# Performance work log

Measured on AMD Instinct MI355X. Metric: run time of the kernel, lower is better.

## Reference

```python
import jax, jax.numpy as jnp
import numpy as np

P_W, P_H = 4, 8            # patch_size=[4,8]: p[0]=width, p[1]=height
EMBED, DEPTH, HEADS = 384, 12, 6
HD = EMBED // HEADS        # 64
THETA = 100.0
LN_EPS = 1e-5


def axial_freqs(pw, ph):
    # compute_axial_cis(dim=HD, end_x=pw, end_y=ph): angles for x and y axes, as cos/sin
    f = 1.0 / THETA ** (np.arange(0, HD, 4)[: HD // 4].astype(np.float32) / HD)  # (16,)
    t = np.arange(pw * ph, dtype=np.float32)
    tx, ty = t % pw, np.floor(t / pw)
    ang = np.concatenate([np.outer(tx, f), np.outer(ty, f)], -1)  # (N, 32)
    return jnp.asarray(np.cos(ang)), jnp.asarray(np.sin(ang))


def patchify(img):
    # (3, h, w) -> (ph*pw, 3*P_H*P_W), matching view/permute in NaViT_ROPE.forward
    c, h, w = img.shape
    ph, pw = h // P_H, w // P_W
    seq = img.reshape(c, ph, P_H, pw, P_W).transpose(1, 3, 0, 2, 4).reshape(ph * pw, -1)
    return seq, ph, pw


def layer_norm(x, w, b):
    m = x.mean(-1, keepdims=True)
    v = ((x - m) ** 2).mean(-1, keepdims=True)
    return (x - m) / jnp.sqrt(v + LN_EPS) * w + b


def rope(x, cos, sin):
    # x: (B,H,N,HD) paired as (...,HD//2,2); cos/sin: (B,N,HD//2)
    xp = x.reshape(*x.shape[:-1], -1, 2)
    x0, x1 = xp[..., 0], xp[..., 1]
    c, s = cos[:, None], sin[:, None]
    return jnp.stack([x0 * c - x1 * s, x0 * s + x1 * c], -1).reshape(x.shape)


def forward(imgs, params):
    (pe_ln_in_w, pe_ln_in_b, pe_w, pe_ln_out_w, pe_ln_out_b, blk, lnf_w, lnf_b) = params
    seqs, coss, sins, lens = [], [], [], []
    for img in imgs:
        seq, ph, pw = patchify(img)
        c, s = axial_freqs(pw, ph)
        seqs.append(seq); coss.append(c); sins.append(s); lens.append(seq.shape[0])
    nmax = max(lens)
    pad = lambda a: jnp.pad(a, ((0, nmax - a.shape[0]), (0, 0)))
    x = jnp.stack([pad(s) for s in seqs])      # (B, Nmax, 96)
    cos = jnp.stack([pad(c) for c in coss])    # (B, Nmax, 32)
    sin = jnp.stack([pad(s) for s in sins])
    mask = jnp.arange(nmax)[None, :] >= jnp.array(lens)[:, None]        # (B, Nmax), True = pad
    attn_bias = jnp.where(mask, -jnp.inf, 0.0)[:, None, None, :]        # (B,1,1,Nmax)

    # patch embed: LN(96) -> Linear(96,384,no bias) -> LN(384)
    x = layer_norm(x, pe_ln_in_w, pe_ln_in_b) @ pe_w
    x = layer_norm(x, pe_ln_out_w, pe_ln_out_b)

    scale = HD ** -0.5

    def block(x, p):
        ln1_w, ln1_b, qkv_w, qkv_b, proj_w, proj_b, ln2_w, ln2_b, fc1_w, fc1_b, fc2_w, fc2_b = p
        B, N, C = x.shape
        h = layer_norm(x, ln1_w, ln1_b)
        qkv = (h @ qkv_w + qkv_b).reshape(B, N, 3, HEADS, HD).transpose(2, 0, 3, 1, 4)
        q, k, v = qkv[0], qkv[1], qkv[2]
        q, k = rope(q, cos, sin), rope(k, cos, sin)
        attn = jnp.einsum('bhnd,bhmd->bhnm', q * scale, k) + attn_bias
        attn = jax.nn.softmax(attn, axis=-1)
        o = jnp.einsum('bhnm,bhmd->bhnd', attn, v).transpose(0, 2, 1, 3).reshape(B, N, C)
        x = x + (o @ proj_w + proj_b)
        h2 = layer_norm(x, ln2_w, ln2_b)
        h2 = jax.nn.gelu(h2 @ fc1_w + fc1_b, approximate=False)  # torch nn.GELU default (erf)
        x = x + (h2 @ fc2_w + fc2_b)
        return x, None

    x, _ = jax.lax.scan(block, x, blk)
    x = layer_norm(x, lnf_w, lnf_b)
    return x, mask


def setup_inputs() -> dict:
    key = jax.random.key(0)
    ks = jax.random.split(key, 10)
    sizes = [(3, 32, 512), (3, 32, 768), (3, 32, 896), (3, 32, 1024)]
    pd = 3 * P_H * P_W  # 96
    w = lambda k, sh: jax.random.normal(k, sh, jnp.float32) * 0.02
    inp = {}
    for i, s in enumerate(sizes):
        inp[f'img{i}'] = jax.random.normal(ks[i], s, jnp.float32)
    inp.update(
        pe_ln_in_w=jnp.ones((pd,), jnp.float32), pe_ln_in_b=jnp.zeros((pd,), jnp.float32),
        pe_w=w(ks[4], (pd, EMBED)),
        pe_ln_out_w=jnp.ones((EMBED,), jnp.float32), pe_ln_out_b=jnp.zeros((EMBED,), jnp.float32),
        ln1_w=jnp.ones((DEPTH, EMBED), jnp.float32), ln1_b=jnp.zeros((DEPTH, EMBED), jnp.float32),
        qkv_w=w(ks[5], (DEPTH, EMBED, 3 * EMBED)), qkv_b=jnp.zeros((DEPTH, 3 * EMBED), jnp.float32),
        proj_w=w(ks[6], (DEPTH, EMBED, EMBED)), proj_b=jnp.zeros((DEPTH, EMBED), jnp.float32),
        ln2_w=jnp.ones((DEPTH, EMBED), jnp.float32), ln2_b=jnp.zeros((DEPTH, EMBED), jnp.float32),
        fc1_w=w(ks[7], (DEPTH, EMBED, 4 * EMBED)), fc1_b=jnp.zeros((DEPTH, 4 * EMBED), jnp.float32),
        fc2_w=w(ks[8], (DEPTH, 4 * EMBED, EMBED)), fc2_b=jnp.zeros((DEPTH, EMBED), jnp.float32),
        lnf_w=jnp.ones((EMBED,), jnp.float32), lnf_b=jnp.zeros((EMBED,), jnp.float32),
    )
    return inp


def reference(img0, img1, img2, img3, pe_ln_in_w, pe_ln_in_b, pe_w, pe_ln_out_w, pe_ln_out_b,
              ln1_w, ln1_b, qkv_w, qkv_b, proj_w, proj_b, ln2_w, ln2_b,
              fc1_w, fc1_b, fc2_w, fc2_b, lnf_w, lnf_b):
    blk = (ln1_w, ln1_b, qkv_w, qkv_b, proj_w, proj_b, ln2_w, ln2_b, fc1_w, fc1_b, fc2_w, fc2_b)
    return forward([img0, img1, img2, img3],
                   (pe_ln_in_w, pe_ln_in_b, pe_w, pe_ln_out_w, pe_ln_out_b, blk, lnf_w, lnf_b))
```

## Files before the change

kernel.cpp:

```cpp
#include <hip/hip_runtime.h>


#define EMBED 384
#define NHEADS 6
#define HD 64
#define NSEQ 1024
#define NB 4
#define NROWS (NB * NSEQ)
#define PD 96
#define NZ 2

typedef __attribute__((ext_vector_type(8))) short bf16x8;
typedef __attribute__((ext_vector_type(4))) float f32x4;

__constant__ int c_lens[4] = {512, 768, 896, 1024};

__device__ __forceinline__ unsigned f2bf(float f) {
    unsigned u = __float_as_uint(f);
    return (u + 0x7fffu + ((u >> 16) & 1u)) >> 16;
}
__device__ __forceinline__ float bf2f(unsigned short h) {
    return __uint_as_float(((unsigned)h) << 16);
}

__global__ void patchify_kernel(const float* __restrict__ i0, const float* __restrict__ i1,
                                const float* __restrict__ i2, const float* __restrict__ i3,
                                float* __restrict__ xin, float* __restrict__ cosT,
                                float* __restrict__ sinT) {
    int bn = blockIdx.x;
    int b = bn >> 10, n = bn & 1023;
    const int lens[4] = {512, 768, 896, 1024};
    const int pws[4]  = {128, 192, 224, 256};
    const float* imgs[4] = {i0, i1, i2, i3};
    int len = lens[b], pw = pws[b];
    int W = pw * 4;
    int t = threadIdx.x;
    float* xrow = xin + (size_t)bn * PD;
    if (n < len) {
        int pr = n / pw, pc = n - pr * pw;
        const float* img = imgs[b];
        if (t < PD) {
            int c = t >> 5, py = (t >> 2) & 7, px = t & 3;
            xrow[t] = img[(size_t)c * 32 * W + (size_t)(pr * 8 + py) * W + pc * 4 + px];
        }
        if (t < 32) {
            int j = t & 15;
            float fr = powf(100.0f, -(float)j / 16.0f);
            float coord = (t < 16) ? (float)pc : (float)pr;
            float ang = coord * fr;
            cosT[(size_t)bn * 32 + t] = cosf(ang);
            sinT[(size_t)bn * 32 + t] = sinf(ang);
        }
    } else {
        if (t < PD) xrow[t] = 0.f;
        if (t < 32) { cosT[(size_t)bn * 32 + t] = 0.f; sinT[(size_t)bn * 32 + t] = 0.f; }
    }
}

__global__ void convT_kernel(const float* __restrict__ src, unsigned short* __restrict__ dst,
                             int K, int N, int Kpad) {
    __shared__ float tile[32][33];
    int k0 = blockIdx.x * 32, n0 = blockIdx.y * 32, l = blockIdx.z;
    int t = threadIdx.x;
    {
        int kk = t >> 3, nn = (t & 7) * 4;
        float4 v = make_float4(0.f, 0.f, 0.f, 0.f);
        if (k0 + kk < K)
            v = *(const float4*)(src + ((size_t)l * K + (k0 + kk)) * N + n0 + nn);
        tile[kk][nn + 0] = v.x; tile[kk][nn + 1] = v.y;
        tile[kk][nn + 2] = v.z; tile[kk][nn + 3] = v.w;
    }
    __syncthreads();
    {
        int nn = t >> 3, kk = (t & 7) * 4;
        unsigned lo = f2bf(tile[kk + 0][nn]) | (f2bf(tile[kk + 1][nn]) << 16);
        unsigned hi = f2bf(tile[kk + 2][nn]) | (f2bf(tile[kk + 3][nn]) << 16);
        uint2 u = make_uint2(lo, hi);
        *(uint2*)(dst + (size_t)l * N * Kpad + (size_t)(n0 + nn) * Kpad + k0 + kk) = u;
    }
}

template <int C, int OS, bool OBF, bool MASK = false>
__global__ void ln_kernel(const float* __restrict__ in, const float* __restrict__ w,
                          const float* __restrict__ bias, void* __restrict__ outv) {
    int row = blockIdx.x * 4 + (threadIdx.x >> 6);
    int t = threadIdx.x & 63;
    const float* x = in + (size_t)row * C;
    constexpr int NE = (C + 63) / 64;
    float vals[NE];
    float s = 0.f;
#pragma unroll
    for (int i = 0; i < NE; i++) {
        int e = t + i * 64;
        float v = (e < C) ? x[e] : 0.f;
        vals[i] = v; s += v;
    }
#pragma unroll
    for (int off = 32; off; off >>= 1) s += __shfl_down(s, off);
    float mean = __shfl(s, 0) / (float)C;
    float vs = 0.f;
#pragma unroll
    for (int i = 0; i < NE; i++) {
        int e = t + i * 64;
        float d = (e < C) ? (vals[i] - mean) : 0.f;
        vs += d * d;
    }
#pragma unroll
    for (int off = 32; off; off >>= 1) vs += __shfl_down(vs, off);
    float rstd = rsqrtf(__shfl(vs, 0) / (float)C + 1e-5f);
    constexpr int NO = (OS + 63) / 64;
#pragma unroll
    for (int i = 0; i < NO; i++) {
        int e = t + i * 64;
        if (e < OS) {
            float v = (e < C) ? ((vals[i] - mean) * rstd * w[e] + bias[e]) : 0.f;
            if (OBF) ((unsigned short*)outv)[(size_t)row * OS + e] = (unsigned short)f2bf(v);
            else     ((float*)outv)[(size_t)row * OS + e] = v;
        }
    }
    if (MASK && t == 0) {
        int b = row >> 10, n = row & 1023;
        ((float*)outv)[(size_t)NROWS * EMBED + row] = (n >= c_lens[b]) ? 1.0f : 0.0f;
    }
}

template <int FLAGS>
__global__ __launch_bounds__(256) void gemm_bf16(
    const unsigned short* __restrict__ A, const unsigned short* __restrict__ Wt,
    const float* __restrict__ bias, const float* __restrict__ res,
    float* __restrict__ outf, unsigned short* __restrict__ outb,
    int M, int K, int N) {
    __shared__ unsigned short As[64][72];
    __shared__ unsigned short Bs[64][72];
    int t = threadIdx.x;
    int wid = t >> 6, lane = t & 63;
    int m0 = blockIdx.y * 64, n0 = blockIdx.x * 64;
    int wm = (wid >> 1) * 32, wn = (wid & 1) * 32;
    f32x4 acc[2][2] = {};
    int srow = t >> 2, sc = (t & 3) * 8;
    const unsigned short* Ap = A + (size_t)(m0 + srow) * K + sc;
    const unsigned short* Bp = Wt + (size_t)(n0 + srow) * K + sc;
    int lr = lane & 15, lk = (lane >> 4) * 8;
    for (int k0 = 0; k0 < K; k0 += 64) {
        *(uint4*)&As[srow][sc]      = *(const uint4*)(Ap + k0);
        *(uint4*)&As[srow][sc + 32] = *(const uint4*)(Ap + k0 + 32);
        *(uint4*)&Bs[srow][sc]      = *(const uint4*)(Bp + k0);
        *(uint4*)&Bs[srow][sc + 32] = *(const uint4*)(Bp + k0 + 32);
        __syncthreads();
#pragma unroll
        for (int kk = 0; kk < 64; kk += 32) {
            bf16x8 a0 = *(const bf16x8*)&As[wm + lr][kk + lk];
            bf16x8 a1 = *(const bf16x8*)&As[wm + 16 + lr][kk + lk];
            bf16x8 b0 = *(const bf16x8*)&Bs[wn + lr][kk + lk];
            bf16x8 b1 = *(const bf16x8*)&Bs[wn + 16 + lr][kk + lk];
            acc[0][0] = __builtin_amdgcn_mfma_f32_16x16x32_bf16(a0, b0, acc[0][0], 0, 0, 0);
            acc[0][1] = __builtin_amdgcn_mfma_f32_16x16x32_bf16(a0, b1, acc[0][1], 0, 0, 0);
            acc[1][0] = __builtin_amdgcn_mfma_f32_16x16x32_bf16(a1, b0, acc[1][0], 0, 0, 0);
            acc[1][1] = __builtin_amdgcn_mfma_f32_16x16x32_bf16(a1, b1, acc[1][1], 0, 0, 0);
        }
        __syncthreads();
    }
    int lq = lane >> 4;
#pragma unroll
    for (int mi = 0; mi < 2; mi++)
#pragma unroll
        for (int ni = 0; ni < 2; ni++) {
#pragma unroll
            for (int r = 0; r < 4; r++) {
                int grow = m0 + wm + mi * 16 + lq * 4 + r;
                int gcol = n0 + wn + ni * 16 + lr;
                float v = acc[mi][ni][r];
                if (FLAGS & 1) v += bias[gcol];
                if (FLAGS & 2) v = 0.5f * v * (1.f + erff(v * 0.70710678118654752f));
                if (FLAGS & 4) v += res[(size_t)grow * N + gcol];
                if (FLAGS & 8) outb[(size_t)grow * N + gcol] = (unsigned short)f2bf(v);
                else           outf[(size_t)grow * N + gcol] = v;
            }
        }
}

template <int FLAGS>
__global__ __launch_bounds__(256) void gemm_bf16_128(
    const unsigned short* __restrict__ A, const unsigned short* __restrict__ Wt,
    const float* __restrict__ bias, const float* __restrict__ res,
    float* __restrict__ outf, unsigned short* __restrict__ outb,
    int M, int K, int N) {
    __shared__ unsigned short As[128][72];
    __shared__ unsigned short Bs[128][72];
    int t = threadIdx.x;
    int wid = t >> 6, lane = t & 63;
    int m0 = blockIdx.y * 128, n0 = blockIdx.x * 128;
    int wm = (wid >> 1) * 64, wn = (wid & 1) * 64;
    f32x4 acc[4][4] = {};
    int srow = t >> 3, sc = (t & 7) * 8;
    const unsigned short* Ap = A + (size_t)(m0 + srow) * K + sc;
    const unsigned short* Bp = Wt + (size_t)(n0 + srow) * K + sc;
    int lr = lane & 15, lk = (lane >> 4) * 8;
    for (int k0 = 0; k0 < K; k0 += 64) {
#pragma unroll
        for (int rr = 0; rr < 4; rr++) {
            *(uint4*)&As[srow + rr * 32][sc] = *(const uint4*)(Ap + (size_t)(rr * 32) * K + k0);
            *(uint4*)&Bs[srow + rr * 32][sc] = *(const uint4*)(Bp + (size_t)(rr * 32) * K + k0);
        }
        __syncthreads();
#pragma unroll
        for (int kk = 0; kk < 64; kk += 32) {
            bf16x8 af[4], bfr[4];
#pragma unroll
            for (int i = 0; i < 4; i++) af[i]  = *(const bf16x8*)&As[wm + i * 16 + lr][kk + lk];
#pragma unroll
            for (int j = 0; j < 4; j++) bfr[j] = *(const bf16x8*)&Bs[wn + j * 16 + lr][kk + lk];
#pragma unroll
            for (int i = 0; i < 4; i++)
#pragma unroll
                for (int j = 0; j < 4; j++)
                    acc[i][j] = __builtin_amdgcn_mfma_f32_16x16x32_bf16(af[i], bfr[j], acc[i][j], 0, 0, 0);
        }
        __syncthreads();
    }
    int lq = lane >> 4;
#pragma unroll
    for (int mi = 0; mi < 4; mi++)
#pragma unroll
        for (int ni = 0; ni < 4; ni++) {
#pragma unroll
            for (int r = 0; r < 4; r++) {
                int grow = m0 + wm + mi * 16 + lq * 4 + r;
                int gcol = n0 + wn + ni * 16 + lr;
                float v = acc[mi][ni][r];
                if (FLAGS & 1) v += bias[gcol];
                if (FLAGS & 2) v = 0.5f * v * (1.f + erff(v * 0.70710678118654752f));
                if (FLAGS & 4) v += res[(size_t)grow * N + gcol];
                if (FLAGS & 8) outb[(size_t)grow * N + gcol] = (unsigned short)f2bf(v);
                else           outf[(size_t)grow * N + gcol] = v;
            }
        }
}

__global__ __launch_bounds__(256) void gemm_qkv_rope(
    const unsigned short* __restrict__ A, const unsigned short* __restrict__ Wt,
    const float* __restrict__ bias, const float* __restrict__ cosT,
    const float* __restrict__ sinT, unsigned short* __restrict__ qr,
    unsigned short* __restrict__ kr, unsigned short* __restrict__ vt) {
    const int K = 384;
    __shared__ unsigned short As[64][72];
    __shared__ unsigned short Bs[64][72];
    int t = threadIdx.x;
    int wid = t >> 6, lane = t & 63;
    int m0 = blockIdx.y * 64, n0 = blockIdx.x * 64;
    int wm = (wid >> 1) * 32, wn = (wid & 1) * 32;
    f32x4 acc[2][2] = {};
    int srow = t >> 2, sc = (t & 3) * 8;
    const unsigned short* Ap = A + (size_t)(m0 + srow) * K + sc;
    const unsigned short* Bp = Wt + (size_t)(n0 + srow) * K + sc;
    int lr = lane & 15, lk = (lane >> 4) * 8;
    for (int k0 = 0; k0 < K; k0 += 64) {
        *(uint4*)&As[srow][sc]      = *(const uint4*)(Ap + k0);
        *(uint4*)&As[srow][sc + 32] = *(const uint4*)(Ap + k0 + 32);
        *(uint4*)&Bs[srow][sc]      = *(const uint4*)(Bp + k0);
        *(uint4*)&Bs[srow][sc + 32] = *(const uint4*)(Bp + k0 + 32);
        __syncthreads();
#pragma unroll
        for (int kk = 0; kk < 64; kk += 32) {
            bf16x8 a0 = *(const bf16x8*)&As[wm + lr][kk + lk];
            bf16x8 a1 = *(const bf16x8*)&As[wm + 16 + lr][kk + lk];
            bf16x8 b0 = *(const bf16x8*)&Bs[wn + lr][kk + lk];
            bf16x8 b1 = *(const bf16x8*)&Bs[wn + 16 + lr][kk + lk];
            acc[0][0] = __builtin_amdgcn_mfma_f32_16x16x32_bf16(a0, b0, acc[0][0], 0, 0, 0);
            acc[0][1] = __builtin_amdgcn_mfma_f32_16x16x32_bf16(a0, b1, acc[0][1], 0, 0, 0);
            acc[1][0] = __builtin_amdgcn_mfma_f32_16x16x32_bf16(a1, b0, acc[1][0], 0, 0, 0);
            acc[1][1] = __builtin_amdgcn_mfma_f32_16x16x32_bf16(a1, b1, acc[1][1], 0, 0, 0);
        }
        __syncthreads();
    }
    int lq = lane >> 4;
    int bx = blockIdx.x;
    int sec = bx / 6, hh = bx - sec * 6;
    if (sec == 2) {
#pragma unroll
        for (int mi = 0; mi < 2; mi++)
#pragma unroll
            for (int ni = 0; ni < 2; ni++) {
                int d = wn + ni * 16 + lr;
                float bb = bias[768 + hh * 64 + d];
                int g0 = m0 + wm + mi * 16 + lq * 4;
                int b = g0 >> 10, n = g0 & 1023;
                uint2 u;
                u.x = f2bf(acc[mi][ni][0] + bb) | (f2bf(acc[mi][ni][1] + bb) << 16);
                u.y = f2bf(acc[mi][ni][2] + bb) | (f2bf(acc[mi][ni][3] + bb) << 16);
                *(uint2*)&vt[((size_t)(b * 6 + hh) * HD + d) * NSEQ + n] = u;
            }
    } else {
        unsigned short* dst = sec ? kr : qr;
        float scl = sec ? 1.0f : 0.125f;
#pragma unroll
        for (int mi = 0; mi < 2; mi++)
#pragma unroll
            for (int ni = 0; ni < 2; ni++) {
                int d = wn + ni * 16 + lr;
                float bb = bias[sec * 384 + hh * 64 + d];
                int pp = d >> 1;
#pragma unroll
                for (int r = 0; r < 4; r++) {
                    int grow = m0 + wm + mi * 16 + lq * 4 + r;
                    float v = acc[mi][ni][r] + bb;
                    float c = cosT[(size_t)grow * 32 + pp];
                    float s = sinT[(size_t)grow * 32 + pp];
                    float vp = __shfl_xor(v, 1);
                    float out = ((d & 1) == 0 ? v * c - vp * s : vp * s + v * c) * scl;
                    int b = grow >> 10, n = grow & 1023;
                    dst[((size_t)(b * 6 + hh) * NSEQ + n) * HD + d] = (unsigned short)f2bf(out);
                }
            }
    }
}

__global__ __launch_bounds__(256) void attn_mfma(
    const unsigned short* __restrict__ qr, const unsigned short* __restrict__ kr,
    const unsigned short* __restrict__ vt, unsigned short* __restrict__ opart,
    float* __restrict__ mP, float* __restrict__ lP) {
    __shared__ unsigned short Ks[64][72];
    __shared__ unsigned short Vs[64][72];
    __shared__ unsigned short Pb[4][16][72];
    __shared__ float Aw[4][16];
    int bh = blockIdx.x;
    int q0 = blockIdx.y * 64;
    int z  = blockIdx.z;
    int len = c_lens[bh / 6];
    int T = len >> 6;
    int t0 = (T * z) >> 1, t1 = (T * (z + 1)) >> 1;
    int t = threadIdx.x, wid = t >> 6, lane = t & 63;
    int lz = lane & 15, lq = lane >> 4;
    const unsigned short* Qp = qr + ((size_t)bh * NSEQ + q0 + wid * 16 + lz) * HD + lq * 8;
    bf16x8 qa0 = *(const bf16x8*)(Qp);
    bf16x8 qa1 = *(const bf16x8*)(Qp + 32);
    int srow = t >> 2, sc = (t & 3) * 16;
    const unsigned short* Kp = kr + (size_t)bh * NSEQ * HD + (size_t)srow * HD + sc;
    const unsigned short* Vp = vt + ((size_t)bh * HD + srow) * NSEQ + sc;
    f32x4 oacc[4] = {};
    float m_s = -1e30f, l_s = 0.f;
    uint4 rk0, rk1, rv0, rv1;
    {
        int k0 = t0 << 6;
        rk0 = *(const uint4*)(Kp + (size_t)k0 * HD);
        rk1 = *(const uint4*)(Kp + (size_t)k0 * HD + 8);
        rv0 = *(const uint4*)(Vp + k0);
        rv1 = *(const uint4*)(Vp + k0 + 8);
    }
    for (int kt = t0; kt < t1; kt++) {
        *(uint4*)&Ks[srow][sc]     = rk0;
        *(uint4*)&Ks[srow][sc + 8] = rk1;
        *(uint4*)&Vs[srow][sc]     = rv0;
        *(uint4*)&Vs[srow][sc + 8] = rv1;
        __syncthreads();
        uint4 nk0, nk1, nv0, nv1;
        if (kt + 1 < t1) {
            int k1 = (kt + 1) << 6;
            nk0 = *(const uint4*)(Kp + (size_t)k1 * HD);
            nk1 = *(const uint4*)(Kp + (size_t)k1 * HD + 8);
            nv0 = *(const uint4*)(Vp + k1);
            nv1 = *(const uint4*)(Vp + k1 + 8);
        }
        f32x4 s[4] = {};
        __builtin_amdgcn_s_setprio(1);
#pragma unroll
        for (int g = 0; g < 4; g++) {
            bf16x8 kf0 = *(const bf16x8*)&Ks[g * 16 + lz][lq * 8];
            bf16x8 kf1 = *(const bf16x8*)&Ks[g * 16 + lz][32 + lq * 8];
            s[g] = __builtin_amdgcn_mfma_f32_16x16x32_bf16(kf0, qa0, s[g], 0, 0, 0);
            s[g] = __builtin_amdgcn_mfma_f32_16x16x32_bf16(kf1, qa1, s[g], 0, 0, 0);
        }
        __builtin_amdgcn_s_setprio(0);
        float mx = s[0][0];
#pragma unroll
        for (int g = 0; g < 4; g++)
#pragma unroll
            for (int r = 0; r < 4; r++) mx = fmaxf(mx, s[g][r]);
        mx = fmaxf(mx, __shfl_xor(mx, 16));
        mx = fmaxf(mx, __shfl_xor(mx, 32));
        float mn = fmaxf(m_s, mx);
        float a_s = __expf(m_s - mn);
        m_s = mn;
        float sum = 0.f;
#pragma unroll
        for (int g = 0; g < 4; g++)
#pragma unroll
            for (int r = 0; r < 4; r++) {
                float p = __expf(s[g][r] - mn);
                s[g][r] = p;
                sum += p;
            }
        sum += __shfl_xor(sum, 16);
        sum += __shfl_xor(sum, 32);
        l_s = l_s * a_s + sum;
        if (lq == 0) Aw[wid][lz] = a_s;
#pragma unroll
        for (int g = 0; g < 4; g++) {
            uint2 u;
            u.x = f2bf(s[g][0]) | (f2bf(s[g][1]) << 16);
            u.y = f2bf(s[g][2]) | (f2bf(s[g][3]) << 16);
            *(uint2*)&Pb[wid][lz][g * 16 + lq * 4] = u;
        }
        f32x4 al4 = *(const f32x4*)&Aw[wid][lq * 4];
        bf16x8 pa0 = *(const bf16x8*)&Pb[wid][lz][lq * 8];
        bf16x8 pa1 = *(const bf16x8*)&Pb[wid][lz][32 + lq * 8];
        __builtin_amdgcn_s_setprio(1);
#pragma unroll
        for (int g = 0; g < 4; g++) {
#pragma unroll
            for (int r = 0; r < 4; r++) oacc[g][r] *= al4[r];
            bf16x8 vf0 = *(const bf16x8*)&Vs[g * 16 + lz][lq * 8];
            bf16x8 vf1 = *(const bf16x8*)&Vs[g * 16 + lz][32 + lq * 8];
            oacc[g] = __builtin_amdgcn_mfma_f32_16x16x32_bf16(pa0, vf0, oacc[g], 0, 0, 0);
            oacc[g] = __builtin_amdgcn_mfma_f32_16x16x32_bf16(pa1, vf1, oacc[g], 0, 0, 0);
        }
        __builtin_amdgcn_s_setprio(0);
        __syncthreads();
        rk0 = nk0; rk1 = nk1; rv0 = nv0; rv1 = nv1;
    }
    size_t rb = ((size_t)z * 24 + bh) * NSEQ + q0 + wid * 16;
    if (lq == 0) { mP[rb + lz] = m_s; lP[rb + lz] = l_s; }
#pragma unroll
    for (int r = 0; r < 4; r++) {
        int row = lq * 4 + r;
#pragma unroll
        for (int g = 0; g < 4; g++)
            opart[(rb + row) * HD + g * 16 + lz] = (unsigned short)f2bf(oacc[g][r]);
    }
}

__global__ __launch_bounds__(256) void gemm_proj_combine(
    const unsigned short* __restrict__ opart, const float* __restrict__ mP,
    const float* __restrict__ lP, const unsigned short* __restrict__ Wt,
    const float* __restrict__ bias, float* __restrict__ xio) {
    const int K = 384, N = 384;
    __shared__ unsigned short As[64][72];
    __shared__ unsigned short Bs[64][72];
    __shared__ float Winv[64][6][NZ];
    int t = threadIdx.x;
    int wid = t >> 6, lane = t & 63;
    int m0 = blockIdx.y * 64, n0 = blockIdx.x * 64;
    int wm = (wid >> 1) * 32, wn = (wid & 1) * 32;
    const size_t zstride = (size_t)24 * NSEQ * HD;
    for (int p = t; p < 384; p += 256) {
        int tok = p / 6, hh = p - tok * 6;
        int g = m0 + tok, b = g >> 10, n = g & 1023;
        int bh = b * 6 + hh;
        size_t i0 = (size_t)bh * NSEQ + n;
        float ma = mP[i0], mb = mP[i0 + (size_t)24 * NSEQ];
        float la = lP[i0], lb = lP[i0 + (size_t)24 * NSEQ];
        float ms = fmaxf(ma, mb);
        float wa = __expf(ma - ms), wb = __expf(mb - ms);
        float inv = 1.f / (la * wa + lb * wb);
        Winv[tok][hh][0] = wa * inv;
        Winv[tok][hh][1] = wb * inv;
    }
    __syncthreads();
    f32x4 acc[2][2] = {};
    int srow = t >> 2, sc = (t & 3) * 8;
    int gg = m0 + srow, gb = gg >> 10, gn = gg & 1023;
    const unsigned short* Bp = Wt + (size_t)(n0 + srow) * K + sc;
    int lr = lane & 15, lk = (lane >> 4) * 8;
    for (int k0 = 0; k0 < K; k0 += 64) {
#pragma unroll
        for (int h = 0; h < 2; h++) {
            int col = k0 + sc + h * 32;
            int hh = col >> 6, d = col & 63;
            int bh = gb * 6 + hh;
            size_t base = ((size_t)bh * NSEQ + gn) * HD + d;
            float w0 = Winv[srow][hh][0], w1 = Winv[srow][hh][1];
            uint4 u0 = *(const uint4*)&opart[base];
            uint4 u1 = *(const uint4*)&opart[base + zstride];
            unsigned a[4] = {u0.x, u0.y, u0.z, u0.w};
            unsigned c[4] = {u1.x, u1.y, u1.z, u1.w};
            uint4 outw;
            unsigned rr[4];
#pragma unroll
            for (int q = 0; q < 4; q++) {
                float lo = bf2f((unsigned short)(a[q] & 0xffff)) * w0 +
                           bf2f((unsigned short)(c[q] & 0xffff)) * w1;
                float hi = bf2f((unsigned short)(a[q] >> 16)) * w0 +
                           bf2f((unsigned short)(c[q] >> 16)) * w1;
                rr[q] = f2bf(lo) | (f2bf(hi) << 16);
            }
            outw.x = rr[0]; outw.y = rr[1]; outw.z = rr[2]; outw.w = rr[3];
            *(uint4*)&As[srow][sc + h * 32] = outw;
        }
        *(uint4*)&Bs[srow][sc]      = *(const uint4*)(Bp + k0);
        *(uint4*)&Bs[srow][sc + 32] = *(const uint4*)(Bp + k0 + 32);
        __syncthreads();
#pragma unroll
        for (int kk = 0; kk < 64; kk += 32) {
            bf16x8 a0 = *(const bf16x8*)&As[wm + lr][kk + lk];
            bf16x8 a1 = *(const bf16x8*)&As[wm + 16 + lr][kk + lk];
            bf16x8 b0 = *(const bf16x8*)&Bs[wn + lr][kk + lk];
            bf16x8 b1 = *(const bf16x8*)&Bs[wn + 16 + lr][kk + lk];
            acc[0][0] = __builtin_amdgcn_mfma_f32_16x16x32_bf16(a0, b0, acc[0][0], 0, 0, 0);
            acc[0][1] = __builtin_amdgcn_mfma_f32_16x16x32_bf16(a0, b1, acc[0][1], 0, 0, 0);
            acc[1][0] = __builtin_amdgcn_mfma_f32_16x16x32_bf16(a1, b0, acc[1][0], 0, 0, 0);
            acc[1][1] = __builtin_amdgcn_mfma_f32_16x16x32_bf16(a1, b1, acc[1][1], 0, 0, 0);
        }
        __syncthreads();
    }
    int lq = lane >> 4;
#pragma unroll
    for (int mi = 0; mi < 2; mi++)
#pragma unroll
        for (int ni = 0; ni < 2; ni++) {
#pragma unroll
            for (int r = 0; r < 4; r++) {
                int grow = m0 + wm + mi * 16 + lq * 4 + r;
                int gcol = n0 + wn + ni * 16 + lr;
                float v = acc[mi][ni][r] + bias[gcol] + xio[(size_t)grow * N + gcol];
                xio[(size_t)grow * N + gcol] = v;
            }
        }
}

extern "C" void kernel_launch(void* const* d_in, const int* in_sizes, int n_in,
                              void* d_out, int out_size, void* d_ws, size_t ws_size,
                              hipStream_t stream) {
    (void)in_sizes; (void)n_in; (void)out_size; (void)ws_size;
    const float* img0 = (const float*)d_in[0];
    const float* img1 = (const float*)d_in[1];
    const float* img2 = (const float*)d_in[2];
    const float* img3 = (const float*)d_in[3];
    const float* pe_ln_in_w  = (const float*)d_in[4];
    const float* pe_ln_in_b  = (const float*)d_in[5];
    const float* pe_w        = (const float*)d_in[6];
    const float* pe_ln_out_w = (const float*)d_in[7];
    const float* pe_ln_out_b = (const float*)d_in[8];
    const float* ln1_w  = (const float*)d_in[9];
    const float* ln1_b  = (const float*)d_in[10];
    const float* qkv_w  = (const float*)d_in[11];
    const float* qkv_b  = (const float*)d_in[12];
    const float* proj_w = (const float*)d_in[13];
    const float* proj_b = (const float*)d_in[14];
    const float* ln2_w  = (const float*)d_in[15];
    const float* ln2_b  = (const float*)d_in[16];
    const float* fc1_w  = (const float*)d_in[17];
    const float* fc1_b  = (const float*)d_in[18];
    const float* fc2_w  = (const float*)d_in[19];
    const float* fc2_b  = (const float*)d_in[20];
    const float* lnf_w  = (const float*)d_in[21];
    const float* lnf_b  = (const float*)d_in[22];

    char* ws = (char*)d_ws;
    float*          x_f    = (float*)(ws + 0);
    char*           R      = ws + 6291456;
    unsigned short* opart  = (unsigned short*)R;
    unsigned short* mlp_bf = (unsigned short*)R;
    unsigned short* h_bf   = (unsigned short*)(ws + 18874368);
    unsigned short* qr     = (unsigned short*)(ws + 22020096);
    unsigned short* kr     = (unsigned short*)(ws + 25165824);
    unsigned short* vt     = (unsigned short*)(ws + 28311552);
    float*          cosT   = (float*)(ws + 31457280);
    float*          sinT   = (float*)(ws + 31981568);
    float*          xin    = (float*)(ws + 32505856);
    float*          mPt    = xin;
    float*          lPt    = (float*)(ws + 32505856 + 393216);
    unsigned short* xln_bf = (unsigned short*)(ws + 34078720);
    unsigned short* pe_wt  = (unsigned short*)(ws + 35127296);
    unsigned short* qkv_wt = (unsigned short*)(ws + 35225600);
    unsigned short* proj_wt= (unsigned short*)(ws + 45842432);
    unsigned short* fc1_wt = (unsigned short*)(ws + 49381376);
    unsigned short* fc2_wt = (unsigned short*)(ws + 63537152);

    convT_kernel<<<dim3(4, 12, 1),   256, 0, stream>>>(pe_w,   pe_wt,   96,  EMBED, 128);
    convT_kernel<<<dim3(12, 36, 12), 256, 0, stream>>>(qkv_w,  qkv_wt,  384, 1152,  384);
    convT_kernel<<<dim3(12, 12, 12), 256, 0, stream>>>(proj_w, proj_wt, 384, 384,   384);
    convT_kernel<<<dim3(12, 48, 12), 256, 0, stream>>>(fc1_w,  fc1_wt,  384, 1536,  384);
    convT_kernel<<<dim3(48, 12, 12), 256, 0, stream>>>(fc2_w,  fc2_wt,  1536, 384,  1536);

    patchify_kernel<<<NROWS, 128, 0, stream>>>(img0, img1, img2, img3, xin, cosT, sinT);
    ln_kernel<PD, 128, true><<<NROWS / 4, 256, 0, stream>>>(xin, pe_ln_in_w, pe_ln_in_b, xln_bf);
    gemm_bf16<0><<<dim3(EMBED / 64, NROWS / 64), 256, 0, stream>>>(
        xln_bf, pe_wt, nullptr, nullptr, x_f, nullptr, NROWS, 128, EMBED);
    ln_kernel<EMBED, EMBED, false><<<NROWS / 4, 256, 0, stream>>>(x_f, pe_ln_out_w, pe_ln_out_b, x_f);

    for (int l = 0; l < 12; ++l) {
        ln_kernel<EMBED, EMBED, true><<<NROWS / 4, 256, 0, stream>>>(
            x_f, ln1_w + l * EMBED, ln1_b + l * EMBED, h_bf);
        gemm_qkv_rope<<<dim3(18, NROWS / 64), 256, 0, stream>>>(
            h_bf, qkv_wt + (size_t)l * 1152 * 384, qkv_b + (size_t)l * 1152,
            cosT, sinT, qr, kr, vt);
        attn_mfma<<<dim3(NB * NHEADS, NSEQ / 64, NZ), 256, 0, stream>>>(
            qr, kr, vt, opart, mPt, lPt);
        gemm_proj_combine<<<dim3(EMBED / 64, NROWS / 64), 256, 0, stream>>>(
            opart, mPt, lPt, proj_wt + (size_t)l * 384 * 384,
            proj_b + (size_t)l * EMBED, x_f);
        ln_kernel<EMBED, EMBED, true><<<NROWS / 4, 256, 0, stream>>>(
            x_f, ln2_w + l * EMBED, ln2_b + l * EMBED, h_bf);
        gemm_bf16_128<11><<<dim3(1536 / 128, NROWS / 128), 256, 0, stream>>>(
            h_bf, fc1_wt + (size_t)l * 1536 * 384, fc1_b + (size_t)l * 1536, nullptr,
            nullptr, mlp_bf, NROWS, EMBED, 1536);
        gemm_bf16<5><<<dim3(EMBED / 64, NROWS / 64), 256, 0, stream>>>(
            mlp_bf, fc2_wt + (size_t)l * 1536 * 384, fc2_b + (size_t)l * EMBED, x_f,
            x_f, nullptr, NROWS, 1536, EMBED);
    }

    ln_kernel<EMBED, EMBED, false, true><<<NROWS / 4, 256, 0, stream>>>(
        x_f, lnf_w, lnf_b, (float*)d_out);
}
```

Before: 1.149 ms.

## Split attention KV range four ways and prefetch GEMM tiles into registers

Raises the attention split-K factor from two to four partitions, so each query tile spreads over more blocks and the proj-combine kernel merges four partial softmax results. It also adds a register prefetch of the next K tile in the generic and QKV GEMMs, overlapping global loads with the MFMA work on the current tile. The trade-off is more partial-output traffic to write and reread in the combine step, plus higher register pressure in the GEMMs.

```diff
diff --git a/kernel.cpp b/kernel.cpp
--- a/kernel.cpp
+++ b/kernel.cpp
@@ -8,7 +8,7 @@
 #define NB 4
 #define NROWS (NB * NSEQ)
 #define PD 96
-#define NZ 2
+#define NZ 4
 
 typedef __attribute__((ext_vector_type(8))) short bf16x8;
 typedef __attribute__((ext_vector_type(4))) float f32x4;
@@ -141,12 +141,22 @@
     const unsigned short* Ap = A + (size_t)(m0 + srow) * K + sc;
     const unsigned short* Bp = Wt + (size_t)(n0 + srow) * K + sc;
     int lr = lane & 15, lk = (lane >> 4) * 8;
+    uint4 ra0 = *(const uint4*)(Ap);
+    uint4 ra1 = *(const uint4*)(Ap + 32);
+    uint4 rb0 = *(const uint4*)(Bp);
+    uint4 rb1 = *(const uint4*)(Bp + 32);
     for (int k0 = 0; k0 < K; k0 += 64) {
-        *(uint4*)&As[srow][sc]      = *(const uint4*)(Ap + k0);
-        *(uint4*)&As[srow][sc + 32] = *(const uint4*)(Ap + k0 + 32);
-        *(uint4*)&Bs[srow][sc]      = *(const uint4*)(Bp + k0);
-        *(uint4*)&Bs[srow][sc + 32] = *(const uint4*)(Bp + k0 + 32);
-        __syncthreads();
+        *(uint4*)&As[srow][sc]      = ra0;
+        *(uint4*)&As[srow][sc + 32] = ra1;
+        *(uint4*)&Bs[srow][sc]      = rb0;
+        *(uint4*)&Bs[srow][sc + 32] = rb1;
+        __syncthreads();
+        if (k0 + 64 < K) {
+            ra0 = *(const uint4*)(Ap + k0 + 64);
+            ra1 = *(const uint4*)(Ap + k0 + 96);
+            rb0 = *(const uint4*)(Bp + k0 + 64);
+            rb1 = *(const uint4*)(Bp + k0 + 96);
+        }
 #pragma unroll
         for (int kk = 0; kk < 64; kk += 32) {
             bf16x8 a0 = *(const bf16x8*)&As[wm + lr][kk + lk];
@@ -254,12 +264,22 @@
     const unsigned short* Ap = A + (size_t)(m0 + srow) * K + sc;
     const unsigned short* Bp = Wt + (size_t)(n0 + srow) * K + sc;
     int lr = lane & 15, lk = (lane >> 4) * 8;
+    uint4 ra0 = *(const uint4*)(Ap);
+    uint4 ra1 = *(const uint4*)(Ap + 32);
+    uint4 rb0 = *(const uint4*)(Bp);
+    uint4 rb1 = *(const uint4*)(Bp + 32);
     for (int k0 = 0; k0 < K; k0 += 64) {
-        *(uint4*)&As[srow][sc]      = *(const uint4*)(Ap + k0);
-        *(uint4*)&As[srow][sc + 32] = *(const uint4*)(Ap + k0 + 32);
-        *(uint4*)&Bs[srow][sc]      = *(const uint4*)(Bp + k0);
-        *(uint4*)&Bs[srow][sc + 32] = *(const uint4*)(Bp + k0 + 32);
-        __syncthreads();
+        *(uint4*)&As[srow][sc]      = ra0;
+        *(uint4*)&As[srow][sc + 32] = ra1;
+        *(uint4*)&Bs[srow][sc]      = rb0;
+        *(uint4*)&Bs[srow][sc + 32] = rb1;
+        __syncthreads();
+        if (k0 + 64 < K) {
+            ra0 = *(const uint4*)(Ap + k0 + 64);
+            ra1 = *(const uint4*)(Ap + k0 + 96);
+            rb0 = *(const uint4*)(Bp + k0 + 64);
+            rb1 = *(const uint4*)(Bp + k0 + 96);
+        }
 #pragma unroll
         for (int kk = 0; kk < 64; kk += 32) {
             bf16x8 a0 = *(const bf16x8*)&As[wm + lr][kk + lk];
@@ -328,7 +348,7 @@
     int z  = blockIdx.z;
     int len = c_lens[bh / 6];
     int T = len >> 6;
-    int t0 = (T * z) >> 1, t1 = (T * (z + 1)) >> 1;
+    int t0 = (T * z) >> 2, t1 = (T * (z + 1)) >> 2;
     int t = threadIdx.x, wid = t >> 6, lane = t & 63;
     int lz = lane & 15, lq = lane >> 4;
     const unsigned short* Qp = qr + ((size_t)bh * NSEQ + q0 + wid * 16 + lz) * HD + lq * 8;
@@ -447,13 +467,20 @@
         int g = m0 + tok, b = g >> 10, n = g & 1023;
         int bh = b * 6 + hh;
         size_t i0 = (size_t)bh * NSEQ + n;
-        float ma = mP[i0], mb = mP[i0 + (size_t)24 * NSEQ];
-        float la = lP[i0], lb = lP[i0 + (size_t)24 * NSEQ];
-        float ms = fmaxf(ma, mb);
-        float wa = __expf(ma - ms), wb = __expf(mb - ms);
-        float inv = 1.f / (la * wa + lb * wb);
-        Winv[tok][hh][0] = wa * inv;
-        Winv[tok][hh][1] = wb * inv;
+        float m[NZ], l[NZ], w[NZ];
+        float ms = -1e30f;
+#pragma unroll
+        for (int z = 0; z < NZ; z++) {
+            m[z] = mP[i0 + (size_t)z * 24 * NSEQ];
+            l[z] = lP[i0 + (size_t)z * 24 * NSEQ];
+            ms = fmaxf(ms, m[z]);
+        }
+        float ls = 0.f;
+#pragma unroll
+        for (int z = 0; z < NZ; z++) { w[z] = __expf(m[z] - ms); ls += l[z] * w[z]; }
+        float inv = 1.f / ls;
+#pragma unroll
+        for (int z = 0; z < NZ; z++) Winv[tok][hh][z] = w[z] * inv;
     }
     __syncthreads();
     f32x4 acc[2][2] = {};
@@ -468,21 +495,24 @@
             int hh = col >> 6, d = col & 63;
             int bh = gb * 6 + hh;
             size_t base = ((size_t)bh * NSEQ + gn) * HD + d;
-            float w0 = Winv[srow][hh][0], w1 = Winv[srow][hh][1];
-            uint4 u0 = *(const uint4*)&opart[base];
-            uint4 u1 = *(const uint4*)&opart[base + zstride];
-            unsigned a[4] = {u0.x, u0.y, u0.z, u0.w};
-            unsigned c[4] = {u1.x, u1.y, u1.z, u1.w};
+            float wz[NZ];
+#pragma unroll
+            for (int z = 0; z < NZ; z++) wz[z] = Winv[srow][hh][z];
+            float lo[4] = {0.f, 0.f, 0.f, 0.f}, hi[4] = {0.f, 0.f, 0.f, 0.f};
+#pragma unroll
+            for (int z = 0; z < NZ; z++) {
+                uint4 u = *(const uint4*)&opart[base + (size_t)z * zstride];
+                unsigned a[4] = {u.x, u.y, u.z, u.w};
+#pragma unroll
+                for (int q = 0; q < 4; q++) {
+                    lo[q] += bf2f((unsigned short)(a[q] & 0xffff)) * wz[z];
+                    hi[q] += bf2f((unsigned short)(a[q] >> 16)) * wz[z];
+                }
+            }
             uint4 outw;
             unsigned rr[4];
 #pragma unroll
-            for (int q = 0; q < 4; q++) {
-                float lo = bf2f((unsigned short)(a[q] & 0xffff)) * w0 +
-                           bf2f((unsigned short)(c[q] & 0xffff)) * w1;
-                float hi = bf2f((unsigned short)(a[q] >> 16)) * w0 +
-                           bf2f((unsigned short)(c[q] >> 16)) * w1;
-                rr[q] = f2bf(lo) | (f2bf(hi) << 16);
-            }
+            for (int q = 0; q < 4; q++) rr[q] = f2bf(lo[q]) | (f2bf(hi[q]) << 16);
             outw.x = rr[0]; outw.y = rr[1]; outw.z = rr[2]; outw.w = rr[3];
             *(uint4*)&As[srow][sc + h * 32] = outw;
         }
```

Result: faster. 1.107 ms (-3.7%).
